# Kernel tuning notes

Hardware: AMD Instinct MI355X
Metric: run time of the kernel (lower is better)

## Reference

```python
import jax, jax.numpy as jnp
import numpy as np

jax.config.update("jax_enable_x64", True)  # loss accumulates int64 squared index diffs (~1e14)

PATCH, STRIDE = 7, 1


def extract_patches(img, p, s):
    # img: [b, c, h, w] -> patches [b, N, c*p*p], N = oh*ow (normalize_patch='none')
    pat = jax.lax.conv_general_dilated_patches(img, (p, p), (s, s), 'VALID')  # [b, c*p*p, oh, ow]
    b, d = pat.shape[0], pat.shape[1]
    return pat.reshape(b, d, -1).transpose(0, 2, 1)


def bisect_left(a, v):
    # Exact replica of np.searchsorted(a, v, side='left') binary search,
    # applied (as in the original code) to an UNSORTED int array `a`.
    # a: [N] int, v: [M] int -> [M] insertion indices in [0, N].
    N = a.shape[0]
    lo = jnp.zeros(v.shape, jnp.int64)
    hi = jnp.full(v.shape, N, jnp.int64)
    n_iter = int(np.ceil(np.log2(N))) + 1
    for _ in range(n_iter):
        mid = (lo + hi) // 2
        am = a[jnp.clip(mid, 0, N - 1)]
        go = lo < hi
        pred = am < v
        lo = jnp.where(go & pred, mid + 1, lo)
        hi = jnp.where(go & (~pred), mid, hi)
    return lo


def nearest_vals(a, v):
    # Vectorized find_nearest(a, v_i) for all v_i. a: [N], v: [M].
    N = a.shape[0]
    idx = bisect_left(a, v)
    a_prev = a[jnp.clip(idx - 1, 0, N - 1)]
    a_at = a[jnp.clip(idx, 0, N - 1)]
    take_prev = (idx > 0) & ((idx == N) | (jnp.abs(v - a_prev) < jnp.abs(v - a_at)))
    return jnp.where(take_prev, a_prev, a_at)


def reference(x, y, rand):
    # rand: [b, d, num_proj]; per-batch projection matrix, normalized by unbiased column std
    rand = rand / jnp.std(rand, axis=1, keepdims=True, ddof=1)
    xp = extract_patches(x, PATCH, STRIDE)  # [b, N, d]
    yp = extract_patches(y, PATCH, STRIDE)  # [b, N, d]
    proj_x = jnp.einsum('bnd,bdp->bnp', xp, rand)
    proj_y = jnp.einsum('bnd,bdp->bnp', yp, rand)
    # Original overwrites projections with argsort indices; only j=0 is used
    # because of the early return inside the projection loop.
    ai = jnp.argsort(proj_x[:, :, 0], axis=1).astype(jnp.int64)  # [b, N]
    at = jnp.argsort(proj_y[:, :, 0], axis=1).astype(jnp.int64)  # [b, N]
    nearest = jax.vmap(nearest_vals)(at, ai)  # [b, N]
    N = ai.shape[1]
    per_image = jnp.sum((ai - nearest) ** 2, axis=1) / N  # int sum -> float
    return jnp.mean(per_image)  # batch_reduction='mean'


def setup_inputs() -> dict:
    key = jax.random.key(0)
    k1, k2, k3 = jax.random.split(key, 3)
    b, c, h, w = 4, 3, 256, 256
    d = c * PATCH * PATCH  # 147
    x = jax.random.normal(k1, (b, c, h, w), dtype=jnp.float32)
    y = jax.random.normal(k2, (b, c, h, w), dtype=jnp.float32)
    rand = jax.random.normal(k3, (b, d, 1), dtype=jnp.float32)
    return {"x": x, "y": y, "rand": rand}
```

## Files before the change

### kernel.cpp

```cpp
#include <hip/hip_runtime.h>
#include <stdint.h>

#define OH 250
#define OW 250
#define NPTS (OH*OW)
#define NSEG 4
#define D 147
#define CH 3
#define IMH 256
#define IMW 256
#define NITER 17
#define NBUCK 8192
#define CAP 128
#define SIG0 12.124355652982141

typedef unsigned long long u64;
typedef unsigned int u32;

#define OFF_SREC  0UL
#define OFF_A     33554432UL
#define OFF_WTS   34554432UL
#define OFF_CURS  34559136UL
#define OFF_BASES 34690208UL
#define OFF_SUMS  34821296UL
#define OFF_TICK  34821328UL
#define OFF_OFLOW 34821336UL
#define WS_NEED   34821340UL

__device__ __forceinline__ u64 packd(double f) {
  u64 u = (u64)__double_as_longlong(f);
  return (u & 0x8000000000000000ULL) ? ~u : (u | 0x8000000000000000ULL);
}

__device__ __forceinline__ int bucket_of(u64 rec) {
  u64 t = rec & ~0x1FFFFULL;
  u64 bits = (t & 0x8000000000000000ULL) ? (t & 0x7FFFFFFFFFFFFFFFULL) : ~t;
  double v = __longlong_as_double((long long)bits);
  double z = (v + 4.0 * SIG0) * ((double)NBUCK / (8.0 * SIG0));
  int b = (z <= 0.0) ? 0 : (int)z;
  if (b > NBUCK - 1) b = NBUCK - 1;
  return b;
}

__global__ __launch_bounds__(256) void setup_kern(const float* __restrict__ rnd,
                                                  double* __restrict__ wts,
                                                  u32* __restrict__ curs,
                                                  u64* __restrict__ sums,
                                                  u32* __restrict__ tick,
                                                  u32* __restrict__ oflow) {
  int t = threadIdx.x;
  if (blockIdx.x < 4) {
    int b = blockIdx.x;
    int lane = t & 63;
    double v0 = (double)rnd[b * D + lane];
    double v1 = (double)rnd[b * D + lane + 64];
    double v2 = (lane + 128 < D) ? (double)rnd[b * D + lane + 128] : 0.0;
    double sm = v0 + v1 + v2;
    #pragma unroll
    for (int o = 32; o > 0; o >>= 1) sm += __shfl_xor(sm, o, 64);
    double mean = sm / (double)D;
    double d0 = v0 - mean, d1 = v1 - mean;
    double d2 = (lane + 128 < D) ? (v2 - mean) : 0.0;
    double ss = d0 * d0 + d1 * d1 + d2 * d2;
    #pragma unroll
    for (int o = 32; o > 0; o >>= 1) ss += __shfl_xor(ss, o, 64);
    double stdv = sqrt(ss / (double)(D - 1));
    if (t < 64) {
      wts[b * D + lane] = v0 / stdv;
      wts[b * D + lane + 64] = v1 / stdv;
      if (lane + 128 < D) wts[b * D + lane + 128] = v2 / stdv;
    }
    if (b == 0 && t < 8) ((u32*)sums)[t] = 0u;
    if (b == 0 && t >= 8 && t < 10) tick[t - 8] = 0u;
    if (b == 0 && t == 10) oflow[0] = 0u;
  } else {
    int g = (blockIdx.x - 4) * 1024 + t * 4;
    if (g < NSEG * NBUCK) {
      curs[g] = 0u; curs[g + 1] = 0u; curs[g + 2] = 0u; curs[g + 3] = 0u;
    }
  }
}

__global__ __launch_bounds__(256) void conv_kern(const float* __restrict__ y,
                                                 const double* __restrict__ wts,
                                                 u64* __restrict__ srec,
                                                 u32* __restrict__ curs,
                                                 u32* __restrict__ oflow) {
  __shared__ float tile[CH][22][22];
  int b = blockIdx.z;
  const float* in = y + (size_t)b * CH * IMH * IMW;
  const double* wb = wts + b * D;
  int bi = blockIdx.y * 16, bj = blockIdx.x * 16;
  int tid = threadIdx.y * 16 + threadIdx.x;
  for (int c = 0; c < CH; ++c)
    for (int t = tid; t < 22 * 22; t += 256) {
      int rr = t / 22, cc = t - rr * 22;
      int r = bi + rr, col = bj + cc;
      float v = 0.f;
      if (r < IMH && col < IMW) v = in[((size_t)c * IMH + r) * IMW + col];
      tile[c][rr][cc] = v;
    }
  __syncthreads();
  int i = bi + threadIdx.y, j = bj + threadIdx.x;
  if (i < OH && j < OW) {
    double acc = 0.0;
    #pragma unroll
    for (int c = 0; c < CH; ++c) {
      double ac = 0.0;
      #pragma unroll
      for (int ph = 0; ph < 7; ++ph)
        #pragma unroll
        for (int pw = 0; pw < 7; ++pw)
          ac = fma((double)tile[c][threadIdx.y + ph][threadIdx.x + pw],
                   wb[c * 49 + ph * 7 + pw], ac);
      acc += ac;
    }
    int n = i * OW + j;
    u64 rec = (packd(acc) & ~0x1FFFFULL) | (u64)(u32)n;
    int bk = b * NBUCK + bucket_of(rec);
    u32 pos = atomicAdd(&curs[bk], 1u);
    if (pos < CAP) srec[(size_t)bk * CAP + pos] = rec;
    else atomicOr(oflow, 1u);
  }
}

__global__ __launch_bounds__(1024) void scan_kern(const u32* __restrict__ curs,
                                                  u32* __restrict__ bases,
                                                  u32* __restrict__ oflow) {
  __shared__ u32 part[1024];
  int seg = blockIdx.x, t = threadIdx.x;
  u32 c[8]; u32 run = 0;
  #pragma unroll
  for (int m = 0; m < 8; ++m) {
    u32 v = curs[seg * NBUCK + 8 * t + m];
    c[m] = v > CAP ? CAP : v;
    run += c[m];
  }
  part[t] = run;
  __syncthreads();
  for (int off = 1; off < 1024; off <<= 1) {
    u32 v = (t >= off) ? part[t - off] : 0u;
    __syncthreads();
    part[t] += v;
    __syncthreads();
  }
  u32 ex = part[t] - run;
  #pragma unroll
  for (int m = 0; m < 8; ++m) {
    bases[seg * (NBUCK + 1) + 8 * t + m] = ex;
    ex += c[m];
  }
  if (t == 1023) {
    bases[seg * (NBUCK + 1) + NBUCK] = ex;
    if (ex != NPTS) atomicOr(oflow, 2u);
  }
}

__global__ __launch_bounds__(512) void bsort_kern(const u64* __restrict__ srec,
                                                  const u32* __restrict__ bases,
                                                  u32* __restrict__ a) {
  __shared__ u64 buf[8][CAP];
  int wid = threadIdx.x >> 6, lane = threadIdx.x & 63;
  int B = blockIdx.x * 8 + wid;
  int seg = B / NBUCK, bk = B & (NBUCK - 1);
  u32 b0 = bases[seg * (NBUCK + 1) + bk];
  u32 b1 = bases[seg * (NBUCK + 1) + bk + 1];
  int n = (int)(b1 - b0);
  const u64* src = srec + (size_t)B * CAP;
  u32* dst = a + (size_t)seg * NPTS + b0;
  for (int i = lane; i < n; i += 64) buf[wid][i] = src[i];
  __syncthreads();
  for (int i = lane; i < n; i += 64) {
    u64 x = buf[wid][i];
    int r = 0;
    for (int j = 0; j < n; ++j) r += (buf[wid][j] < x);
    dst[r] = (u32)(x & 0x1FFFFULL);
  }
}

#define HALF (NSEG * NPTS / 2)
__global__ __launch_bounds__(256) void loss_kern(const u32* __restrict__ a_all,
                                                 u64* __restrict__ sums,
                                                 u32* __restrict__ tick,
                                                 const u32* __restrict__ oflow,
                                                 float* __restrict__ out,
                                                 int nblocks) {
  __shared__ u64 lsums[NSEG];
  __shared__ u32 rank_s;
  int tid = threadIdx.x;
  if (tid < NSEG) lsums[tid] = 0ULL;
  __syncthreads();
  int g = blockIdx.x * 256 + tid;
  if (g < HALF) {
    int g1 = g + HALF;
    int s0 = g / NPTS, s1 = g1 / NPTS;
    int vv0 = g - s0 * NPTS, vv1 = g1 - s1 * NPTS;
    const u32* A0 = a_all + (size_t)s0 * NPTS;
    const u32* A1 = a_all + (size_t)s1 * NPTS;
    int lo0 = 0, hi0 = NPTS, lo1 = 0, hi1 = NPTS;
    #pragma unroll
    for (int it = 0; it < NITER; ++it) {
      int mid0 = (lo0 + hi0) >> 1, mid1 = (lo1 + hi1) >> 1;
      int cm0 = mid0 > NPTS - 1 ? NPTS - 1 : mid0;
      int cm1 = mid1 > NPTS - 1 ? NPTS - 1 : mid1;
      int am0 = (int)A0[cm0];
      int am1 = (int)A1[cm1];
      if (lo0 < hi0) { if (am0 < vv0) lo0 = mid0 + 1; else hi0 = mid0; }
      if (lo1 < hi1) { if (am1 < vv1) lo1 = mid1 + 1; else hi1 = mid1; }
    }
    {
      int pi = lo0 - 1; if (pi < 0) pi = 0; if (pi > NPTS - 1) pi = NPTS - 1;
      int ci = lo0;     if (ci > NPTS - 1) ci = NPTS - 1;
      int ap = (int)A0[pi], aa = (int)A0[ci];
      int d1 = vv0 - ap; if (d1 < 0) d1 = -d1;
      int d2 = vv0 - aa; if (d2 < 0) d2 = -d2;
      bool tp = (lo0 > 0) && ((lo0 == NPTS) || (d1 < d2));
      long long dd = (long long)(vv0 - (tp ? ap : aa));
      atomicAdd(&lsums[s0], (u64)(dd * dd));
    }
    {
      int pi = lo1 - 1; if (pi < 0) pi = 0; if (pi > NPTS - 1) pi = NPTS - 1;
      int ci = lo1;     if (ci > NPTS - 1) ci = NPTS - 1;
      int ap = (int)A1[pi], aa = (int)A1[ci];
      int d1 = vv1 - ap; if (d1 < 0) d1 = -d1;
      int d2 = vv1 - aa; if (d2 < 0) d2 = -d2;
      bool tp = (lo1 > 0) && ((lo1 == NPTS) || (d1 < d2));
      long long dd = (long long)(vv1 - (tp ? ap : aa));
      atomicAdd(&lsums[s1], (u64)(dd * dd));
    }
  }
  __syncthreads();
  if (tid < NSEG && lsums[tid]) atomicAdd(&sums[tid], lsums[tid]);
  __syncthreads();
  if (tid == 0) {
    rank_s = atomicAdd(&tick[1], 1u);
    if (rank_s == (u32)(nblocks - 1)) {
      u32 of = __hip_atomic_load(oflow, __ATOMIC_RELAXED, __HIP_MEMORY_SCOPE_AGENT);
      if (of) { out[0] = 8.0e12f + 1.0e11f * (float)of; return; }
      double l = 0.0;
      for (int s = 0; s < NSEG; ++s) {
        u64 sv = __hip_atomic_load(&sums[s], __ATOMIC_RELAXED, __HIP_MEMORY_SCOPE_AGENT);
        l += (double)(long long)sv / (double)NPTS;
      }
      out[0] = (float)(l / 4.0);
    }
  }
}

__global__ void guard_kern(float* __restrict__ out) {
  if (threadIdx.x == 0 && blockIdx.x == 0) out[0] = 9.0e12f;
}

extern "C" void kernel_launch(void* const* d_in, const int* in_sizes, int n_in,
                              void* d_out, int out_size, void* d_ws, size_t ws_size,
                              hipStream_t stream) {
  (void)in_sizes; (void)n_in; (void)out_size;
  if (ws_size < WS_NEED) { guard_kern<<<1, 64, 0, stream>>>((float*)d_out); return; }
  const float* y   = (const float*)d_in[1];
  const float* rnd = (const float*)d_in[2];

  char* ws = (char*)d_ws;
  u64* srec   = (u64*)(ws + OFF_SREC);
  u32* aidx   = (u32*)(ws + OFF_A);
  double* wts = (double*)(ws + OFF_WTS);
  u32* curs   = (u32*)(ws + OFF_CURS);
  u32* bases  = (u32*)(ws + OFF_BASES);
  u64* sums   = (u64*)(ws + OFF_SUMS);
  u32* tick   = (u32*)(ws + OFF_TICK);
  u32* oflow  = (u32*)(ws + OFF_OFLOW);
  float* out  = (float*)d_out;

  setup_kern<<<36, 256, 0, stream>>>(rnd, wts, curs, sums, tick, oflow);
  conv_kern<<<dim3(16, 16, NSEG), dim3(16, 16), 0, stream>>>(y, wts, srec, curs, oflow);
  scan_kern<<<NSEG, 1024, 0, stream>>>(curs, bases, oflow);
  bsort_kern<<<NSEG * NBUCK / 8, 512, 0, stream>>>(srec, bases, aidx);
  int nb = (HALF + 255) / 256;
  loss_kern<<<nb, 256, 0, stream>>>(aidx, sums, tick, oflow, out, nb);
}
```

Baseline: 118.4 us.

## Fuse bucket scan into conv via last-block ticket and shuffle-based bucket sort

```diff
diff --git a/kernel.cpp b/kernel.cpp
--- a/kernel.cpp
+++ b/kernel.cpp
@@ -13,6 +13,7 @@
 #define NBUCK 8192
 #define CAP 128
 #define SIG0 12.124355652982141
+#define CONV_BLOCKS (16*16*NSEG)
 
 typedef unsigned long long u64;
 typedef unsigned int u32;
@@ -85,8 +86,12 @@
                                                  const double* __restrict__ wts,
                                                  u64* __restrict__ srec,
                                                  u32* __restrict__ curs,
+                                                 u32* __restrict__ bases,
+                                                 u32* __restrict__ tick,
                                                  u32* __restrict__ oflow) {
   __shared__ float tile[CH][22][22];
+  __shared__ u32 wsum[4];
+  __shared__ u32 scanflag;
   int b = blockIdx.z;
   const float* in = y + (size_t)b * CH * IMH * IMW;
   const double* wb = wts + b * D;
@@ -122,59 +127,90 @@
     if (pos < CAP) srec[(size_t)bk * CAP + pos] = rec;
     else atomicOr(oflow, 1u);
   }
-}
-
-__global__ __launch_bounds__(1024) void scan_kern(const u32* __restrict__ curs,
-                                                  u32* __restrict__ bases,
-                                                  u32* __restrict__ oflow) {
-  __shared__ u32 part[1024];
-  int seg = blockIdx.x, t = threadIdx.x;
-  u32 c[8]; u32 run = 0;
-  #pragma unroll
-  for (int m = 0; m < 8; ++m) {
-    u32 v = curs[seg * NBUCK + 8 * t + m];
-    c[m] = v > CAP ? CAP : v;
-    run += c[m];
-  }
-  part[t] = run;
-  __syncthreads();
-  for (int off = 1; off < 1024; off <<= 1) {
-    u32 v = (t >= off) ? part[t - off] : 0u;
-    __syncthreads();
-    part[t] += v;
-    __syncthreads();
-  }
-  u32 ex = part[t] - run;
-  #pragma unroll
-  for (int m = 0; m < 8; ++m) {
-    bases[seg * (NBUCK + 1) + 8 * t + m] = ex;
-    ex += c[m];
-  }
-  if (t == 1023) {
-    bases[seg * (NBUCK + 1) + NBUCK] = ex;
-    if (ex != NPTS) atomicOr(oflow, 2u);
-  }
-}
-
-__global__ __launch_bounds__(512) void bsort_kern(const u64* __restrict__ srec,
+  __syncthreads();
+  if (tid == 0) {
+    u32 r = atomicAdd(&tick[0], 1u);
+    scanflag = (r == (u32)(CONV_BLOCKS - 1)) ? 1u : 0u;
+  }
+  __syncthreads();
+  if (scanflag) {
+    int lane = tid & 63, wid = tid >> 6;
+    int base = tid * 32;
+    for (int seg = 0; seg < NSEG; ++seg) {
+      const u32* cs = curs + seg * NBUCK;
+      u32 run = 0;
+      for (int m = 0; m < 32; ++m) {
+        u32 v = __hip_atomic_load(&cs[base + m], __ATOMIC_RELAXED, __HIP_MEMORY_SCOPE_AGENT);
+        run += (v > CAP ? CAP : v);
+      }
+      u32 inc = run;
+      #pragma unroll
+      for (int o = 1; o < 64; o <<= 1) {
+        u32 v = __shfl_up(inc, o, 64);
+        if (lane >= o) inc += v;
+      }
+      if (lane == 63) wsum[wid] = inc;
+      __syncthreads();
+      u32 woff = 0;
+      for (int w2 = 0; w2 < wid; ++w2) woff += wsum[w2];
+      u32 ex = woff + inc - run;
+      u32* bs = bases + seg * (NBUCK + 1);
+      for (int m = 0; m < 32; ++m) {
+        u32 v = __hip_atomic_load(&cs[base + m], __ATOMIC_RELAXED, __HIP_MEMORY_SCOPE_AGENT);
+        v = (v > CAP ? CAP : v);
+        bs[base + m] = ex;
+        ex += v;
+      }
+      if (tid == 255) {
+        bs[NBUCK] = ex;
+        if (ex != NPTS) atomicOr(oflow, 2u);
+      }
+      __syncthreads();
+    }
+  }
+}
+
+__global__ __launch_bounds__(256) void bsort_kern(const u64* __restrict__ srec,
                                                   const u32* __restrict__ bases,
                                                   u32* __restrict__ a) {
-  __shared__ u64 buf[8][CAP];
   int wid = threadIdx.x >> 6, lane = threadIdx.x & 63;
-  int B = blockIdx.x * 8 + wid;
-  int seg = B / NBUCK, bk = B & (NBUCK - 1);
-  u32 b0 = bases[seg * (NBUCK + 1) + bk];
-  u32 b1 = bases[seg * (NBUCK + 1) + bk + 1];
-  int n = (int)(b1 - b0);
-  const u64* src = srec + (size_t)B * CAP;
-  u32* dst = a + (size_t)seg * NPTS + b0;
-  for (int i = lane; i < n; i += 64) buf[wid][i] = src[i];
-  __syncthreads();
-  for (int i = lane; i < n; i += 64) {
-    u64 x = buf[wid][i];
-    int r = 0;
-    for (int j = 0; j < n; ++j) r += (buf[wid][j] < x);
-    dst[r] = (u32)(x & 0x1FFFFULL);
+  int wg = blockIdx.x * 4 + wid;
+  int B0 = wg * 4;
+  int seg = B0 >> 13;
+  int bk0 = B0 & (NBUCK - 1);
+  const u32* bb = bases + seg * (NBUCK + 1) + bk0;
+  u32 b[5];
+  #pragma unroll
+  for (int k = 0; k < 5; ++k) b[k] = bb[k];
+  int n[4]; u64 r0[4], r1[4];
+  #pragma unroll
+  for (int k = 0; k < 4; ++k) {
+    n[k] = (int)(b[k + 1] - b[k]);
+    const u64* src = srec + (size_t)(B0 + k) * CAP;
+    r0[k] = (lane < n[k]) ? src[lane] : ~0ULL;
+    r1[k] = (lane + 64 < n[k]) ? src[lane + 64] : ~0ULL;
+  }
+  u32* aseg = a + (size_t)seg * NPTS;
+  #pragma unroll
+  for (int k = 0; k < 4; ++k) {
+    int nk = n[k];
+    if (nk <= 0) continue;
+    u64 x0 = r0[k], x1 = r1[k];
+    int rk0 = 0, rk1 = 0;
+    int n0 = nk < 64 ? nk : 64;
+    for (int j = 0; j < n0; ++j) {
+      u64 bj = __shfl(x0, j, 64);
+      rk0 += (bj < x0);
+      rk1 += (bj < x1);
+    }
+    for (int j = 64; j < nk; ++j) {
+      u64 bj = __shfl(x1, j - 64, 64);
+      rk0 += (bj < x0);
+      rk1 += (bj < x1);
+    }
+    u32* dst = aseg + b[k];
+    if (lane < nk) dst[rk0] = (u32)(x0 & 0x1FFFFULL);
+    if (lane + 64 < nk) dst[rk1] = (u32)(x1 & 0x1FFFFULL);
   }
 }
 
@@ -271,9 +307,9 @@
   float* out  = (float*)d_out;
 
   setup_kern<<<36, 256, 0, stream>>>(rnd, wts, curs, sums, tick, oflow);
-  conv_kern<<<dim3(16, 16, NSEG), dim3(16, 16), 0, stream>>>(y, wts, srec, curs, oflow);
-  scan_kern<<<NSEG, 1024, 0, stream>>>(curs, bases, oflow);
-  bsort_kern<<<NSEG * NBUCK / 8, 512, 0, stream>>>(srec, bases, aidx);
+  conv_kern<<<dim3(16, 16, NSEG), dim3(16, 16), 0, stream>>>(y, wts, srec, curs, bases,
+                                                             tick, oflow);
+  bsort_kern<<<2048, 256, 0, stream>>>(srec, bases, aidx);
   int nb = (HALF + 255) / 256;
   loss_kern<<<nb, 256, 0, stream>>>(aidx, sums, tick, oflow, out, nb);
 }
```

Result: slower. 182.5 us (+54.2%).
